# Performance work log

Hardware: AMD Instinct MI355X
Metric: run time of the kernel (lower is better)

## Reference

```python
import jax, jax.numpy as jnp
import numpy as np

N_NODES = 50000


def _gcn_norm(edge_index, num_nodes):
    # PyG GCNConv default: add self-loops, symmetric deg^{-1/2} normalization.
    src, dst = edge_index[0], edge_index[1]
    loops = jnp.arange(num_nodes, dtype=src.dtype)
    src = jnp.concatenate([src, loops])
    dst = jnp.concatenate([dst, loops])
    ones = jnp.ones(src.shape[0], dtype=jnp.float32)
    deg = jax.ops.segment_sum(ones, dst, num_segments=num_nodes)
    dinv = jnp.where(deg > 0, jax.lax.rsqrt(deg), 0.0)
    norm = dinv[src] * dinv[dst]  # [E + N]
    return src, dst, norm


def _gcn_layer(x, src, dst, norm, W, b, num_nodes):
    h = x @ W                                   # [N, H]
    msg = h[src] * norm[:, None]                # gather + scale, [E+N, H]
    out = jax.ops.segment_sum(msg, dst, num_segments=num_nodes)  # scatter-add
    return out + b


def setup_inputs() -> dict:
    key = jax.random.key(0)
    ks = jax.random.split(key, 8)
    d_in, d_h = 128, 128
    x = jax.random.normal(ks[0], (N_NODES, d_in), dtype=jnp.float32)
    edge_index = jax.random.randint(ks[1], (2, 800000), 0, N_NODES, dtype=jnp.int64)
    s1 = 1.0 / np.sqrt(d_in)
    s2 = 1.0 / np.sqrt(d_h)
    W1 = jax.random.normal(ks[2], (d_in, d_h), dtype=jnp.float32) * s1
    b1 = jnp.zeros((d_h,), dtype=jnp.float32)
    W2 = jax.random.normal(ks[3], (d_h, d_h), dtype=jnp.float32) * s2
    b2 = jnp.zeros((d_h,), dtype=jnp.float32)
    Wl = jax.random.normal(ks[4], (d_h, 1), dtype=jnp.float32) * s2
    bl = jnp.zeros((1,), dtype=jnp.float32)
    return {"x": x, "edge_index": edge_index, "W1": W1, "b1": b1,
            "W2": W2, "b2": b2, "Wl": Wl, "bl": bl}


def reference(x, edge_index, W1, b1, W2, b2, Wl, bl):
    n = x.shape[0]
    src, dst, norm = _gcn_norm(edge_index, n)
    h = jax.nn.relu(_gcn_layer(x, src, dst, norm, W1, b1, n))
    # dropout is identity in eval mode
    h = _gcn_layer(h, src, dst, norm, W2, b2, n)
    return jax.nn.sigmoid(h @ Wl + bl)  # [N, 1]
```

## Files before the change

kernel.cpp:

```cpp
#include <hip/hip_runtime.h>
#include <math.h>

#define NN 50000
#define NE 800000
#define DD 128
#define NPAD 50048
#define NSLICE 6256
#define ELLW 64

typedef __attribute__((ext_vector_type(8))) short bf16x8;
typedef __attribute__((ext_vector_type(4))) float f32x4;
typedef __attribute__((ext_vector_type(2))) float f32x2;

__device__ __forceinline__ int clampN(int v) {
  return v < 0 ? 0 : (v >= NN ? NN - 1 : v);
}

__device__ __forceinline__ unsigned short f2b(float f) {
  union { float f; unsigned int u; } x; x.f = f;
  unsigned int u = x.u;
  u += 0x7fffu + ((u >> 16) & 1u);
  return (unsigned short)(u >> 16);
}

__device__ __forceinline__ float blo(unsigned int v) {
  union { unsigned int u; float f; } a; a.u = v << 16; return a.f;
}
__device__ __forceinline__ float bhi(unsigned int v) {
  union { unsigned int u; float f; } a; a.u = v & 0xffff0000u; return a.f;
}


__global__ __launch_bounds__(256) void k_prep_w(
    const float* __restrict__ W1, const float* __restrict__ W2,
    const float* __restrict__ b2, const float* __restrict__ Wl,
    const float* __restrict__ bl, unsigned short* __restrict__ Wt1,
    float* __restrict__ w2l, float* __restrict__ c0b) {
  __shared__ float part[2];
  if (blockIdx.x < 64) {
    int i = blockIdx.x * 256 + threadIdx.x;
    int n = i >> 7, k = i & 127;
    Wt1[i] = f2b(W1[k * DD + n]);
  } else if (threadIdx.x < DD) {
    int k = threadIdx.x;
    float acc = 0.f;
    for (int c = 0; c < DD; ++c) acc += W2[k * DD + c] * Wl[c];
    w2l[k] = acc;
    float pc = b2[k] * Wl[k];
#pragma unroll
    for (int off = 32; off > 0; off >>= 1) pc += __shfl_down(pc, off, 64);
    if ((k & 63) == 0) part[k >> 6] = pc;
    __syncthreads();
    if (k == 0) c0b[0] = part[0] + part[1] + bl[0];
  }
}


__device__ __forceinline__ void scat1(int d, int s, int lo, int hi,
                                      int* __restrict__ cur,
                                      unsigned short* __restrict__ col) {
  if (d >= lo && d < hi) {
    int pos = atomicAdd(&cur[d], 1);
    if (pos < ELLW) col[d * ELLW + pos] = (unsigned short)clampN(s);
  }
}

__global__ __launch_bounds__(256) void k_scatter4(
    const int4* __restrict__ src4, const int4* __restrict__ dst4,
    int* __restrict__ cur, unsigned short* __restrict__ col) {
  int g = blockIdx.x & 7;
  int blk = blockIdx.x >> 3;
  int lo = g * NSLICE;
  int hi = min(lo + NSLICE, NN);
  const int n4 = NE / 4;
  for (int i = blk * 256 + threadIdx.x; i < n4; i += 256 * 256) {
    int4 d4 = dst4[i];
    d4.x = clampN(d4.x); d4.y = clampN(d4.y);
    d4.z = clampN(d4.z); d4.w = clampN(d4.w);
    bool any = (d4.x >= lo && d4.x < hi) | (d4.y >= lo && d4.y < hi) |
               (d4.z >= lo && d4.z < hi) | (d4.w >= lo && d4.w < hi);
    if (any) {
      int4 s4 = src4[i];
      scat1(d4.x, s4.x, lo, hi, cur, col);
      scat1(d4.y, s4.y, lo, hi, cur, col);
      scat1(d4.z, s4.z, lo, hi, cur, col);
      scat1(d4.w, s4.w, lo, hi, cur, col);
    }
  }
}

__global__ void k_dinv(const int* __restrict__ cur, float* __restrict__ dinv, int n) {
  int i = blockIdx.x * blockDim.x + threadIdx.x;
  if (i < n) dinv[i] = rsqrtf(1.0f + (float)cur[i]);
}


__global__ __launch_bounds__(256) void k_gemm_f32(
    const float* __restrict__ x, const unsigned short* __restrict__ Wt,
    const float* __restrict__ dinv, unsigned short* __restrict__ outb) {
  __shared__ char lds[16384 + 32768];
  char* Al = lds;
  char* Wl = lds + 16384;

  const int tid = threadIdx.x;
  const int row0 = blockIdx.x * 64;

  {
    const float4* src = (const float4*)x;
#pragma unroll
    for (int kk = 0; kk < 8; ++kk) {
      int idx = tid + kk * 256;
      int r = idx >> 5;
      int c4 = idx & 31;
      float4 v = make_float4(0.f, 0.f, 0.f, 0.f);
      if (row0 + r < NN) v = src[(size_t)(row0 + r) * 32 + c4];
      ushort4 u;
      u.x = f2b(v.x); u.y = f2b(v.y); u.z = f2b(v.z); u.w = f2b(v.w);
      int bo = r * 256 + c4 * 8;
      *(ushort4*)(Al + (bo ^ ((r & 7) << 4))) = u;
    }
  }
  {
    const uint4* src = (const uint4*)Wt;
    for (int idx = tid; idx < 2048; idx += 256) {
      int bo = idx * 16;
      int r = bo >> 8;
      *(uint4*)(Wl + (bo ^ ((r & 7) << 4))) = src[idx];
    }
  }
  __syncthreads();

  const int w = tid >> 6, lane = tid & 63;
  const int lr = lane & 15, lk = lane >> 4;

  bf16x8 af[4];
  {
    int ar = w * 16 + lr;
    int base = ar * 256 + lk * 16;
    int swz = (ar & 7) << 4;
#pragma unroll
    for (int k4 = 0; k4 < 4; ++k4)
      af[k4] = *(const bf16x8*)(Al + ((base + k4 * 64) ^ swz));
  }

  f32x4 accs[8];
#pragma unroll
  for (int n = 0; n < 8; ++n) {
    f32x4 acc = {0.f, 0.f, 0.f, 0.f};
    int br = n * 16 + lr;
    int bbase = br * 256 + lk * 16;
    int bswz = (br & 7) << 4;
#pragma unroll
    for (int k4 = 0; k4 < 4; ++k4) {
      bf16x8 bf = *(const bf16x8*)(Wl + ((bbase + k4 * 64) ^ bswz));
      acc = __builtin_amdgcn_mfma_f32_16x16x32_bf16(af[k4], bf, acc, 0, 0, 0);
    }
    accs[n] = acc;
  }

#pragma unroll
  for (int r = 0; r < 4; ++r) {
    int grow = row0 + w * 16 + lk * 4 + r;
    if (grow < NN) {
      float dv = dinv[grow];
#pragma unroll
      for (int n = 0; n < 8; ++n)
        outb[(size_t)grow * DD + n * 16 + lr] = f2b(accs[n][r] * dv);
    }
  }
}


__device__ __forceinline__ void accp(f32x2* acc, uint4 v) {
  f32x2 a0 = {blo(v.x), bhi(v.x)};
  f32x2 a1 = {blo(v.y), bhi(v.y)};
  f32x2 a2 = {blo(v.z), bhi(v.z)};
  f32x2 a3 = {blo(v.w), bhi(v.w)};
  acc[0] += a0;
  acc[1] += a1;
  acc[2] += a2;
  acc[3] += a3;
}

__global__ __launch_bounds__(256) void k_agg_relu_proj_ell(
    const uint4* __restrict__ tpb4, const float* __restrict__ dinv,
    const float* __restrict__ b, const float* __restrict__ w2l,
    const int* __restrict__ cur, const unsigned short* __restrict__ col,
    float* __restrict__ s_out) {
  int wid = threadIdx.x >> 6;
  int lane = threadIdx.x & 63;
  int d = blockIdx.x * 4 + wid;
  int il = lane & 7, g = lane >> 3;

  f32x2 acc[8];
#pragma unroll
  for (int j = 0; j < 8; ++j) acc[j] = (f32x2){0.f, 0.f};

  int deg = min(cur[d], ELLW);
  const unsigned short* crow = col + d * ELLW;
  for (int e = g; e < deg; e += 8) {
    int s = crow[e];
    uint4 v0 = tpb4[(size_t)s * 16 + il * 2];
    uint4 v1 = tpb4[(size_t)s * 16 + il * 2 + 1];
    accp(acc, v0);
    accp(acc + 4, v1);
  }
#pragma unroll
  for (int j = 0; j < 8; ++j) {
    float ax = acc[j].x, ay = acc[j].y;
    ax += __shfl_xor(ax, 8, 64);  ay += __shfl_xor(ay, 8, 64);
    ax += __shfl_xor(ax, 16, 64); ay += __shfl_xor(ay, 16, 64);
    ax += __shfl_xor(ax, 32, 64); ay += __shfl_xor(ay, 32, 64);
    acc[j].x = ax; acc[j].y = ay;
  }
  uint4 s0 = tpb4[(size_t)d * 16 + il * 2];
  uint4 s1 = tpb4[(size_t)d * 16 + il * 2 + 1];
  accp(acc, s0);
  accp(acc + 4, s1);

  float dv = dinv[d];
  float p = 0.f;
#pragma unroll
  for (int q = 0; q < 4; ++q) {
    float4 bb = ((const float4*)b)[il * 4 + q];
    float4 ww = ((const float4*)w2l)[il * 4 + q];
    p = fmaf(fmaxf(fmaf(dv, acc[2 * q].x, bb.x), 0.f), ww.x, p);
    p = fmaf(fmaxf(fmaf(dv, acc[2 * q].y, bb.y), 0.f), ww.y, p);
    p = fmaf(fmaxf(fmaf(dv, acc[2 * q + 1].x, bb.z), 0.f), ww.z, p);
    p = fmaf(fmaxf(fmaf(dv, acc[2 * q + 1].y, bb.w), 0.f), ww.w, p);
  }
  p += __shfl_xor(p, 1, 64);
  p += __shfl_xor(p, 2, 64);
  p += __shfl_xor(p, 4, 64);
  if (lane == 0) s_out[d] = dv * p;
}


__global__ __launch_bounds__(256) void k_agg_scalar_ell(
    const float* __restrict__ s, const float* __restrict__ dinv,
    const float* __restrict__ c0b, const int* __restrict__ cur,
    const unsigned short* __restrict__ col, float* __restrict__ out) {
  int wid = threadIdx.x >> 6;
  int lane = threadIdx.x & 63;
  int q = lane & 15;
  int d = blockIdx.x * 16 + wid * 4 + (lane >> 4);

  int deg = min(cur[d], ELLW);
  const unsigned short* crow = col + d * ELLW;
  float tot = 0.f;
  for (int e = q; e < deg; e += 16) tot += s[crow[e]];
  tot += __shfl_xor(tot, 1, 64);
  tot += __shfl_xor(tot, 2, 64);
  tot += __shfl_xor(tot, 4, 64);
  tot += __shfl_xor(tot, 8, 64);
  if (q == 0) {
    float z = dinv[d] * (tot + s[d]) + c0b[0];
    out[d] = 1.f / (1.f + expf(-z));
  }
}


extern "C" void kernel_launch(void* const* d_in, const int* in_sizes, int n_in,
                              void* d_out, int out_size, void* d_ws, size_t ws_size,
                              hipStream_t stream) {
  const float* x = (const float*)d_in[0];
  const int* ei = (const int*)d_in[1];
  const float* W1 = (const float*)d_in[2];
  const float* b1 = (const float*)d_in[3];
  const float* W2 = (const float*)d_in[4];
  const float* b2 = (const float*)d_in[5];
  const float* Wl = (const float*)d_in[6];
  const float* bl = (const float*)d_in[7];
  float* out = (float*)d_out;

  char* ws = (char*)d_ws;
  size_t off = 0;
  auto alloc = [&](size_t bytes) -> char* {
    char* p = ws + off;
    off = (off + bytes + 255) & ~(size_t)255;
    return p;
  };
  int* cur = (int*)alloc(NN * sizeof(int));
  float* dinv = (float*)alloc(NN * sizeof(float));
  unsigned short* colell = (unsigned short*)alloc((size_t)NN * ELLW * 2);
  unsigned short* Wt1 = (unsigned short*)alloc(DD * DD * 2);
  float* w2l = (float*)alloc(DD * sizeof(float));
  float* c0b = (float*)alloc(sizeof(float));
  unsigned short* tpb = (unsigned short*)alloc((size_t)NPAD * DD * 2);
  float* sbuf = (float*)alloc(NN * sizeof(float));
  (void)ws_size;

  const int NB_N = (NN + 255) / 256;

  hipMemsetAsync(cur, 0, NN * sizeof(int), stream);
  k_prep_w<<<65, 256, 0, stream>>>(W1, W2, b2, Wl, bl, Wt1, w2l, c0b);

  k_scatter4<<<2048, 256, 0, stream>>>((const int4*)ei, (const int4*)(ei + NE),
                                       cur, colell);
  k_dinv<<<NB_N, 256, 0, stream>>>(cur, dinv, NN);

  k_gemm_f32<<<NPAD / 64, 256, 0, stream>>>(x, Wt1, dinv, tpb);

  k_agg_relu_proj_ell<<<NN / 4, 256, 0, stream>>>((const uint4*)tpb, dinv, b1, w2l,
                                                  cur, colell, sbuf);
  k_agg_scalar_ell<<<(NN + 15) / 16, 256, 0, stream>>>(sbuf, dinv, c0b, cur,
                                                       colell, out);
}
```

Baseline: 120.5 us.

## Fold memset and dinv into other kernels, flatten scatter with nontemporal stores

Replaces the memset with extra blocks in the weight-prep kernel that zero the degree counters. The separate dinv kernel is removed, and rsqrt(1+deg) is recomputed inline wherever it is needed. The 8-way destination-sliced scatter becomes a single flat pass using nontemporal stores for the ELL column writes. This cuts two launches and the repeated edge reads, but loses the locality that slicing gave the atomics and column writes.

After: 127.7 us. +6.0%, slower.

```diff
diff --git a/kernel.cpp b/kernel.cpp
--- a/kernel.cpp
+++ b/kernel.cpp
@@ -5,7 +5,6 @@
 #define NE 800000
 #define DD 128
 #define NPAD 50048
-#define NSLICE 6256
 #define ELLW 64
 
 typedef __attribute__((ext_vector_type(8))) short bf16x8;
@@ -35,69 +34,58 @@
     const float* __restrict__ W1, const float* __restrict__ W2,
     const float* __restrict__ b2, const float* __restrict__ Wl,
     const float* __restrict__ bl, unsigned short* __restrict__ Wt1,
-    float* __restrict__ w2l, float* __restrict__ c0b) {
+    float* __restrict__ w2l, float* __restrict__ c0b, int* __restrict__ cur) {
   __shared__ float part[2];
   if (blockIdx.x < 64) {
     int i = blockIdx.x * 256 + threadIdx.x;
     int n = i >> 7, k = i & 127;
     Wt1[i] = f2b(W1[k * DD + n]);
-  } else if (threadIdx.x < DD) {
-    int k = threadIdx.x;
-    float acc = 0.f;
-    for (int c = 0; c < DD; ++c) acc += W2[k * DD + c] * Wl[c];
-    w2l[k] = acc;
-    float pc = b2[k] * Wl[k];
-#pragma unroll
-    for (int off = 32; off > 0; off >>= 1) pc += __shfl_down(pc, off, 64);
-    if ((k & 63) == 0) part[k >> 6] = pc;
-    __syncthreads();
-    if (k == 0) c0b[0] = part[0] + part[1] + bl[0];
-  }
-}
-
-
-__device__ __forceinline__ void scat1(int d, int s, int lo, int hi,
-                                      int* __restrict__ cur,
+  } else if (blockIdx.x == 64) {
+    if (threadIdx.x < DD) {
+      int k = threadIdx.x;
+      float acc = 0.f;
+      for (int c = 0; c < DD; ++c) acc += W2[k * DD + c] * Wl[c];
+      w2l[k] = acc;
+      float pc = b2[k] * Wl[k];
+#pragma unroll
+      for (int off = 32; off > 0; off >>= 1) pc += __shfl_down(pc, off, 64);
+      if ((k & 63) == 0) part[k >> 6] = pc;
+      __syncthreads();
+      if (k == 0) c0b[0] = part[0] + part[1] + bl[0];
+    }
+  } else {
+    int i = (blockIdx.x - 65) * 256 + threadIdx.x;
+    if (i < NN) cur[i] = 0;
+  }
+}
+
+
+__device__ __forceinline__ void scat1(int d, int s, int* __restrict__ cur,
                                       unsigned short* __restrict__ col) {
-  if (d >= lo && d < hi) {
-    int pos = atomicAdd(&cur[d], 1);
-    if (pos < ELLW) col[d * ELLW + pos] = (unsigned short)clampN(s);
-  }
-}
-
-__global__ __launch_bounds__(256) void k_scatter4(
+  d = clampN(d);
+  int pos = atomicAdd(&cur[d], 1);
+  if (pos < ELLW)
+    __builtin_nontemporal_store((unsigned short)clampN(s), &col[d * ELLW + pos]);
+}
+
+__global__ __launch_bounds__(256) void k_scatter_nt(
     const int4* __restrict__ src4, const int4* __restrict__ dst4,
     int* __restrict__ cur, unsigned short* __restrict__ col) {
-  int g = blockIdx.x & 7;
-  int blk = blockIdx.x >> 3;
-  int lo = g * NSLICE;
-  int hi = min(lo + NSLICE, NN);
-  const int n4 = NE / 4;
-  for (int i = blk * 256 + threadIdx.x; i < n4; i += 256 * 256) {
+  int i = blockIdx.x * 256 + threadIdx.x;
+  if (i < NE / 4) {
     int4 d4 = dst4[i];
-    d4.x = clampN(d4.x); d4.y = clampN(d4.y);
-    d4.z = clampN(d4.z); d4.w = clampN(d4.w);
-    bool any = (d4.x >= lo && d4.x < hi) | (d4.y >= lo && d4.y < hi) |
-               (d4.z >= lo && d4.z < hi) | (d4.w >= lo && d4.w < hi);
-    if (any) {
-      int4 s4 = src4[i];
-      scat1(d4.x, s4.x, lo, hi, cur, col);
-      scat1(d4.y, s4.y, lo, hi, cur, col);
-      scat1(d4.z, s4.z, lo, hi, cur, col);
-      scat1(d4.w, s4.w, lo, hi, cur, col);
-    }
-  }
-}
-
-__global__ void k_dinv(const int* __restrict__ cur, float* __restrict__ dinv, int n) {
-  int i = blockIdx.x * blockDim.x + threadIdx.x;
-  if (i < n) dinv[i] = rsqrtf(1.0f + (float)cur[i]);
+    int4 s4 = src4[i];
+    scat1(d4.x, s4.x, cur, col);
+    scat1(d4.y, s4.y, cur, col);
+    scat1(d4.z, s4.z, cur, col);
+    scat1(d4.w, s4.w, cur, col);
+  }
 }
 
 
 __global__ __launch_bounds__(256) void k_gemm_f32(
     const float* __restrict__ x, const unsigned short* __restrict__ Wt,
-    const float* __restrict__ dinv, unsigned short* __restrict__ outb) {
+    const int* __restrict__ cur, unsigned short* __restrict__ outb) {
   __shared__ char lds[16384 + 32768];
   char* Al = lds;
   char* Wl = lds + 16384;
@@ -162,7 +150,7 @@
   for (int r = 0; r < 4; ++r) {
     int grow = row0 + w * 16 + lk * 4 + r;
     if (grow < NN) {
-      float dv = dinv[grow];
+      float dv = rsqrtf(1.0f + (float)cur[grow]);
 #pragma unroll
       for (int n = 0; n < 8; ++n)
         outb[(size_t)grow * DD + n * 16 + lr] = f2b(accs[n][r] * dv);
@@ -183,10 +171,9 @@
 }
 
 __global__ __launch_bounds__(256) void k_agg_relu_proj_ell(
-    const uint4* __restrict__ tpb4, const float* __restrict__ dinv,
-    const float* __restrict__ b, const float* __restrict__ w2l,
-    const int* __restrict__ cur, const unsigned short* __restrict__ col,
-    float* __restrict__ s_out) {
+    const uint4* __restrict__ tpb4, const float* __restrict__ b,
+    const float* __restrict__ w2l, const int* __restrict__ cur,
+    const unsigned short* __restrict__ col, float* __restrict__ s_out) {
   int wid = threadIdx.x >> 6;
   int lane = threadIdx.x & 63;
   int d = blockIdx.x * 4 + wid;
@@ -196,7 +183,8 @@
 #pragma unroll
   for (int j = 0; j < 8; ++j) acc[j] = (f32x2){0.f, 0.f};
 
-  int deg = min(cur[d], ELLW);
+  int degd = cur[d];
+  int deg = min(degd, ELLW);
   const unsigned short* crow = col + d * ELLW;
   for (int e = g; e < deg; e += 8) {
     int s = crow[e];
@@ -218,7 +206,7 @@
   accp(acc, s0);
   accp(acc + 4, s1);
 
-  float dv = dinv[d];
+  float dv = rsqrtf(1.0f + (float)degd);
   float p = 0.f;
 #pragma unroll
   for (int q = 0; q < 4; ++q) {
@@ -237,15 +225,16 @@
 
 
 __global__ __launch_bounds__(256) void k_agg_scalar_ell(
-    const float* __restrict__ s, const float* __restrict__ dinv,
-    const float* __restrict__ c0b, const int* __restrict__ cur,
-    const unsigned short* __restrict__ col, float* __restrict__ out) {
+    const float* __restrict__ s, const float* __restrict__ c0b,
+    const int* __restrict__ cur, const unsigned short* __restrict__ col,
+    float* __restrict__ out) {
   int wid = threadIdx.x >> 6;
   int lane = threadIdx.x & 63;
   int q = lane & 15;
   int d = blockIdx.x * 16 + wid * 4 + (lane >> 4);
 
-  int deg = min(cur[d], ELLW);
+  int degd = cur[d];
+  int deg = min(degd, ELLW);
   const unsigned short* crow = col + d * ELLW;
   float tot = 0.f;
   for (int e = q; e < deg; e += 16) tot += s[crow[e]];
@@ -254,7 +243,8 @@
   tot += __shfl_xor(tot, 4, 64);
   tot += __shfl_xor(tot, 8, 64);
   if (q == 0) {
-    float z = dinv[d] * (tot + s[d]) + c0b[0];
+    float dv = rsqrtf(1.0f + (float)degd);
+    float z = dv * (tot + s[d]) + c0b[0];
     out[d] = 1.f / (1.f + expf(-z));
   }
 }
@@ -281,7 +271,6 @@
     return p;
   };
   int* cur = (int*)alloc(NN * sizeof(int));
-  float* dinv = (float*)alloc(NN * sizeof(float));
   unsigned short* colell = (unsigned short*)alloc((size_t)NN * ELLW * 2);
   unsigned short* Wt1 = (unsigned short*)alloc(DD * DD * 2);
   float* w2l = (float*)alloc(DD * sizeof(float));
@@ -290,19 +279,14 @@
   float* sbuf = (float*)alloc(NN * sizeof(float));
   (void)ws_size;
 
-  const int NB_N = (NN + 255) / 256;
-
-  hipMemsetAsync(cur, 0, NN * sizeof(int), stream);
-  k_prep_w<<<65, 256, 0, stream>>>(W1, W2, b2, Wl, bl, Wt1, w2l, c0b);
-
-  k_scatter4<<<2048, 256, 0, stream>>>((const int4*)ei, (const int4*)(ei + NE),
-                                       cur, colell);
-  k_dinv<<<NB_N, 256, 0, stream>>>(cur, dinv, NN);
-
-  k_gemm_f32<<<NPAD / 64, 256, 0, stream>>>(x, Wt1, dinv, tpb);
-
-  k_agg_relu_proj_ell<<<NN / 4, 256, 0, stream>>>((const uint4*)tpb, dinv, b1, w2l,
+  k_prep_w<<<65 + 196, 256, 0, stream>>>(W1, W2, b2, Wl, bl, Wt1, w2l, c0b, cur);
+
+  k_scatter_nt<<<(NE / 4 + 255) / 256, 256, 0, stream>>>(
+      (const int4*)ei, (const int4*)(ei + NE), cur, colell);
+
+  k_gemm_f32<<<NPAD / 64, 256, 0, stream>>>(x, Wt1, cur, tpb);
+
+  k_agg_relu_proj_ell<<<NN / 4, 256, 0, stream>>>((const uint4*)tpb, b1, w2l,
                                                   cur, colell, sbuf);
-  k_agg_scalar_ell<<<(NN + 15) / 16, 256, 0, stream>>>(sbuf, dinv, c0b, cur,
-                                                       colell, out);
-}
+  k_agg_scalar_ell<<<(NN + 15) / 16, 256, 0, stream>>>(sbuf, c0b, cur, colell, out);
+}
```
